# Kernel optimization log

Measured on AMD Instinct MI355X. Metric: run time of the kernel, lower is better.

The kernel has to match this reference:

```python
import jax, jax.numpy as jnp
import numpy as np

N, E, D_IN, D_HID, D_OUT = 50000, 800000, 64, 128, 64


def setup_inputs() -> dict:
    key = jax.random.key(0)
    ks = jax.random.split(key, 8)
    x = jax.random.normal(ks[0], (N, D_IN), dtype=jnp.float32)
    edge_index = jax.random.randint(ks[1], (2, E), 0, N, dtype=jnp.int64)
    # SAGEConv layer 1: lin_l (agg path, with bias), lin_r (root path, no bias)
    s1 = 1.0 / np.sqrt(D_IN)
    W_l1 = jax.random.uniform(ks[2], (D_HID, D_IN), jnp.float32, -s1, s1)
    b_l1 = jnp.zeros((D_HID,), jnp.float32)
    W_r1 = jax.random.uniform(ks[3], (D_HID, D_IN), jnp.float32, -s1, s1)
    s2 = 1.0 / np.sqrt(D_HID)
    W_l2 = jax.random.uniform(ks[4], (D_OUT, D_HID), jnp.float32, -s2, s2)
    b_l2 = jnp.zeros((D_OUT,), jnp.float32)
    W_r2 = jax.random.uniform(ks[5], (D_OUT, D_HID), jnp.float32, -s2, s2)
    return {"x": x, "edge_index": edge_index,
            "W_l1": W_l1, "b_l1": b_l1, "W_r1": W_r1,
            "W_l2": W_l2, "b_l2": b_l2, "W_r2": W_r2}


def _sage_layer(h, src, dst, W_l, b_l, W_r, n_nodes):
    # scatter-mean of source features onto targets
    msg = h[src]                                               # [E, d]
    summed = jax.ops.segment_sum(msg, dst, num_segments=n_nodes)
    deg = jax.ops.segment_sum(jnp.ones((src.shape[0], 1), h.dtype), dst,
                              num_segments=n_nodes)
    agg = summed / jnp.maximum(deg, 1.0)                       # [n, d]
    return agg @ W_l.T + b_l + h @ W_r.T


def reference(x, edge_index, W_l1, b_l1, W_r1, W_l2, b_l2, W_r2):
    src, dst = edge_index[0], edge_index[1]
    n = x.shape[0]
    h = _sage_layer(x, src, dst, W_l1, b_l1, W_r1, n)
    h = jnp.tanh(h)
    h = _sage_layer(h, src, dst, W_l2, b_l2, W_r2, n)
    return jax.nn.log_softmax(h, axis=1)
```

## Files before the change

### kernel.cpp

```cpp
#include <hip/hip_runtime.h>
#include <hip/hip_bf16.h>
#include <math.h>


typedef unsigned short u16;
typedef unsigned int   u32;
typedef __attribute__((ext_vector_type(8))) __bf16 bf16x8;
typedef __attribute__((ext_vector_type(4))) float  f32x4;

__device__ __forceinline__ u16 f2bf(float f) {
    u32 u = __float_as_uint(f);
    u32 r = (u + 0x7FFFu + ((u >> 16) & 1u)) >> 16;
    return (u16)r;
}
__device__ __forceinline__ float bfl(u32 u) { return __uint_as_float(u << 16); }
__device__ __forceinline__ float bfh(u32 u) { return __uint_as_float(u & 0xFFFF0000u); }
__device__ __forceinline__ u32 pack2(float a, float b) {
    return (u32)f2bf(a) | ((u32)f2bf(b) << 16);
}
__device__ __forceinline__ int pad16(int x) { return (x + 15) & ~15; }

__device__ __forceinline__ void fill_body(
    const int* __restrict__ src, const int* __restrict__ dst,
    int* __restrict__ cnt, u16* __restrict__ perm, int E, int N8,
    float invN8, int vb, int tid)
{
    int g = vb & 7;
    int e0 = (vb >> 3) * 2048 + tid * 8;
    int d[8];
    if (e0 + 8 <= E) {
        int4 d0 = *(const int4*)(dst + e0);
        int4 d1 = *(const int4*)(dst + e0 + 4);
        d[0] = d0.x; d[1] = d0.y; d[2] = d0.z; d[3] = d0.w;
        d[4] = d1.x; d[5] = d1.y; d[6] = d1.z; d[7] = d1.w;
    } else {
        for (int k = 0; k < 8; k++) d[k] = (e0 + k < E) ? dst[e0 + k] : -1;
    }
#pragma unroll
    for (int k = 0; k < 8; k++) {
        int dd = d[k];
        if (dd < 0) continue;
        int b = (int)((float)dd * invN8);
        if (dd >= (b + 1) * N8) b++;
        else if (dd < b * N8) b--;
        if (b != g) continue;
        int pos = atomicAdd(&cnt[dd], 1);
        if (pos < 64) perm[(size_t)dd * 64 + pos] = (u16)src[e0 + k];
    }
}

__global__ __launch_bounds__(256) void prep_kernel(
    const int* __restrict__ src, const int* __restrict__ dst,
    int* __restrict__ cnt, u16* __restrict__ perm, int E, int N8, float invN8,
    const float* __restrict__ x, uint4* __restrict__ xb4, int nCvt8,
    const float* __restrict__ Wl1, const float* __restrict__ Wr1,
    const float* __restrict__ Wl2, const float* __restrict__ Wr2,
    u16* __restrict__ W1c, u16* __restrict__ W2c,
    u16* __restrict__ xb, u16* __restrict__ m2b,
    int N, int FB, int VB)
{
    int blk = blockIdx.x, tid = threadIdx.x;
    if (blk < FB) {
        fill_body(src, dst, cnt, perm, E, N8, invN8, blk, tid);
    } else if (blk < FB + VB) {
        int i = (blk - FB) * 256 + tid;
        if (i < nCvt8) {
            float4 v0 = ((const float4*)x)[i * 2];
            float4 v1 = ((const float4*)x)[i * 2 + 1];
            uint4 p;
            p.x = pack2(v0.x, v0.y); p.y = pack2(v0.z, v0.w);
            p.z = pack2(v1.x, v1.y); p.w = pack2(v1.z, v1.w);
            xb4[i] = p;
        }
    } else if (blk < FB + VB + 64) {
        int i = (blk - FB - VB) * 256 + tid;
        if (i < 128 * 128) {
            int o = i >> 7, k = i & 127;
            float w1 = (k < 64) ? Wr1[o * 64 + k] : Wl1[o * 64 + (k - 64)];
            W1c[i] = f2bf(w1);
            float w2 = (o < 64) ? Wl2[o * 128 + k] : Wr2[(o - 64) * 128 + k];
            W2c[i] = f2bf(w2);
        }
    } else {
        if (tid < 32)      ((u32*)(xb  + (size_t)N * 64))[tid] = 0;
        else if (tid < 64) ((u32*)(m2b + (size_t)N * 64))[tid - 32] = 0;
    }
}

__device__ __forceinline__ void gather_wide(
    const u32* __restrict__ feat2, const u16* __restrict__ perm,
    int slot0, int degc, int pd, int rg, int c8, int lane, int N,
    float acc[8])
{
    float accB[8];
#pragma unroll
    for (int k = 0; k < 8; k++) { acc[k] = 0.f; accB[k] = 0.f; }
    int pidx = (int)perm[slot0 + lane];
    pidx = (lane < degc) ? pidx : N;
    for (int j = 0; j < pd; j += 16) {
        int rA = __shfl(pidx, j + rg,     64);
        int rB = __shfl(pidx, j + 8 + rg, 64);
        uint4 uA = *(const uint4*)(feat2 + (size_t)rA * 32 + c8 * 4);
        uint4 uB = *(const uint4*)(feat2 + (size_t)rB * 32 + c8 * 4);
        acc[0] += bfl(uA.x); acc[1] += bfh(uA.x);
        acc[2] += bfl(uA.y); acc[3] += bfh(uA.y);
        acc[4] += bfl(uA.z); acc[5] += bfh(uA.z);
        acc[6] += bfl(uA.w); acc[7] += bfh(uA.w);
        accB[0] += bfl(uB.x); accB[1] += bfh(uB.x);
        accB[2] += bfl(uB.y); accB[3] += bfh(uB.y);
        accB[4] += bfl(uB.z); accB[5] += bfh(uB.z);
        accB[6] += bfl(uB.w); accB[7] += bfh(uB.w);
    }
#pragma unroll
    for (int k = 0; k < 8; k++) acc[k] += accB[k];
#pragma unroll
    for (int k = 0; k < 8; k++) {
        acc[k] += __shfl_xor(acc[k], 8, 64);
        acc[k] += __shfl_xor(acc[k], 16, 64);
        acc[k] += __shfl_xor(acc[k], 32, 64);
    }
}

__global__ __launch_bounds__(512, 4) void gather_layer12_kernel(
    const u16* __restrict__ xb, const u16* __restrict__ perm,
    const int* __restrict__ cnt,
    const u16* __restrict__ W1, const float* __restrict__ b1,
    const u16* __restrict__ W2, const float* __restrict__ b2,
    u16* __restrict__ m2b, float* __restrict__ out, int N)
{
    __shared__ u16 agg_lds[64 * 64];
    __shared__ u16 tile4[4 * 2048];
    const int tid = threadIdx.x;
    const int wv = tid >> 6, lane = tid & 63;
    const int tb = blockIdx.x;

    {
        const int rg = lane >> 3, c8 = lane & 7;
#pragma unroll 2
        for (int i = 0; i < 8; i++) {
            int rr = wv * 8 + i;
            int nodec = min(tb * 64 + rr, N - 1);
            int deg = cnt[nodec];
            int degc = min(deg, 64);
            int pd = pad16(degc);
            float acc[8];
            gather_wide((const u32*)xb, perm, nodec * 64, degc, pd,
                        rg, c8, lane, N, acc);
            if (rg == 0) {
                float inv = 1.f / fmaxf((float)deg, 1.f);
                uint4 p;
                p.x = pack2(acc[0] * inv, acc[1] * inv);
                p.y = pack2(acc[2] * inv, acc[3] * inv);
                p.z = pack2(acc[4] * inv, acc[5] * inv);
                p.w = pack2(acc[6] * inv, acc[7] * inv);
                *(uint4*)&agg_lds[rr * 64 + ((c8 ^ (rr & 7)) << 3)] = p;
            }
        }
    }
    __syncthreads();

    const int quad = lane >> 4, l16 = lane & 15;
    u16* tile = tile4 + wv * 2048;
    bf16x8 a0, a1, a2, a3;
    if (wv < 4) {
        int node = tb * 64 + wv * 16 + l16;
        int nclamp = min(node, N - 1);
        const u16* xrow = xb + (size_t)nclamp * 64;
        a0 = *(const bf16x8*)(xrow + quad * 8);
        a1 = *(const bf16x8*)(xrow + 32 + quad * 8);
        int rr = wv * 16 + l16;
        a2 = *(const bf16x8*)&agg_lds[rr * 64 + ((quad       ^ (rr & 7)) << 3)];
        a3 = *(const bf16x8*)&agg_lds[rr * 64 + (((quad + 4) ^ (rr & 7)) << 3)];
#pragma unroll
        for (int nt = 0; nt < 8; nt++) {
            const u16* wrow = W1 + (size_t)(nt * 16 + l16) * 128 + quad * 8;
            f32x4 acc = {0.f, 0.f, 0.f, 0.f};
            acc = __builtin_amdgcn_mfma_f32_16x16x32_bf16(a0, *(const bf16x8*)(wrow),      acc, 0, 0, 0);
            acc = __builtin_amdgcn_mfma_f32_16x16x32_bf16(a1, *(const bf16x8*)(wrow + 32), acc, 0, 0, 0);
            acc = __builtin_amdgcn_mfma_f32_16x16x32_bf16(a2, *(const bf16x8*)(wrow + 64), acc, 0, 0, 0);
            acc = __builtin_amdgcn_mfma_f32_16x16x32_bf16(a3, *(const bf16x8*)(wrow + 96), acc, 0, 0, 0);
            int col = nt * 16 + l16;
            float bias = b1[col];
#pragma unroll
            for (int r = 0; r < 4; r++) {
                int row = quad * 4 + r;
                tile[row * 128 + (col ^ ((row & 7) << 3))] =
                    f2bf(tanhf(acc[r] + bias));
            }
        }
    }
    __syncthreads();

    if (wv < 4) {
        int swz = (l16 & 7) << 3;
        bf16x8 h0 = *(const bf16x8*)&tile[l16 * 128 + (( 0 + quad * 8) ^ swz)];
        bf16x8 h1 = *(const bf16x8*)&tile[l16 * 128 + ((32 + quad * 8) ^ swz)];
        bf16x8 h2 = *(const bf16x8*)&tile[l16 * 128 + ((64 + quad * 8) ^ swz)];
        bf16x8 h3 = *(const bf16x8*)&tile[l16 * 128 + ((96 + quad * 8) ^ swz)];
        int orow = tb * 64 + wv * 16 + quad * 4;
#pragma unroll
        for (int nt = 0; nt < 8; nt++) {
            const u16* wrow = W2 + (size_t)(nt * 16 + l16) * 128 + quad * 8;
            f32x4 acc = {0.f, 0.f, 0.f, 0.f};
            acc = __builtin_amdgcn_mfma_f32_16x16x32_bf16(h0, *(const bf16x8*)(wrow),      acc, 0, 0, 0);
            acc = __builtin_amdgcn_mfma_f32_16x16x32_bf16(h1, *(const bf16x8*)(wrow + 32), acc, 0, 0, 0);
            acc = __builtin_amdgcn_mfma_f32_16x16x32_bf16(h2, *(const bf16x8*)(wrow + 64), acc, 0, 0, 0);
            acc = __builtin_amdgcn_mfma_f32_16x16x32_bf16(h3, *(const bf16x8*)(wrow + 96), acc, 0, 0, 0);
            int oc = nt * 16 + l16;
#pragma unroll
            for (int r = 0; r < 4; r++) {
                int nn = orow + r;
                if (nn >= N) continue;
                if (oc < 64) m2b[(size_t)nn * 64 + oc] = f2bf(acc[r]);
                else         out[(size_t)nn * 64 + (oc - 64)] = acc[r] + b2[oc - 64];
            }
        }
    }
}

__global__ __launch_bounds__(256, 4) void gather2_final_kernel(
    const u32* __restrict__ m2b2, const u16* __restrict__ perm,
    const int* __restrict__ cnt, float* __restrict__ out, int N)
{
    int wid  = blockIdx.x * 4 + (threadIdx.x >> 6);
    int lane = threadIdx.x & 63;
    if (wid >= N) return;
    int deg = cnt[wid];
    int degc = min(deg, 64);
    int pd = pad16(degc);
    int rg = lane >> 3, c8 = lane & 7;
    float acc[8];
    gather_wide(m2b2, perm, wid * 64, degc, pd, rg, c8, lane, N, acc);
    float inv = 1.f / fmaxf((float)deg, 1.f);
    const float4* orow = (const float4*)(out + (size_t)wid * 64);
    float4 r20 = orow[c8 * 2];
    float4 r21 = orow[c8 * 2 + 1];
    float v[8];
    v[0] = acc[0] * inv + r20.x; v[1] = acc[1] * inv + r20.y;
    v[2] = acc[2] * inv + r20.z; v[3] = acc[3] * inv + r20.w;
    v[4] = acc[4] * inv + r21.x; v[5] = acc[5] * inv + r21.y;
    v[6] = acc[6] * inv + r21.z; v[7] = acc[7] * inv + r21.w;
    float m = v[0];
#pragma unroll
    for (int k = 1; k < 8; k++) m = fmaxf(m, v[k]);
#pragma unroll
    for (int o = 1; o < 8; o <<= 1) m = fmaxf(m, __shfl_xor(m, o, 64));
    float s = 0.f;
#pragma unroll
    for (int k = 0; k < 8; k++) s += expf(v[k] - m);
#pragma unroll
    for (int o = 1; o < 8; o <<= 1) s += __shfl_xor(s, o, 64);
    if (rg == 0) {
        float ls = m + logf(s);
        float4* ow = (float4*)(out + (size_t)wid * 64);
        ow[c8 * 2]     = make_float4(v[0] - ls, v[1] - ls, v[2] - ls, v[3] - ls);
        ow[c8 * 2 + 1] = make_float4(v[4] - ls, v[5] - ls, v[6] - ls, v[7] - ls);
    }
}

extern "C" void kernel_launch(void* const* d_in, const int* in_sizes, int n_in,
                              void* d_out, int out_size, void* d_ws, size_t ws_size,
                              hipStream_t stream)
{
    const float* x   = (const float*)d_in[0];
    const int*   ei  = (const int*)d_in[1];
    const float* Wl1 = (const float*)d_in[2];
    const float* bl1 = (const float*)d_in[3];
    const float* Wr1 = (const float*)d_in[4];
    const float* Wl2 = (const float*)d_in[5];
    const float* bl2 = (const float*)d_in[6];
    const float* Wr2 = (const float*)d_in[7];
    float* out = (float*)d_out;

    int N = in_sizes[0] / 64;
    int E = in_sizes[1] / 2;
    const int* src = ei;
    const int* dst = ei + E;
    int N8 = (N + 7) / 8;
    float invN8 = 1.0f / (float)N8;
    int chunks = (E + 2047) / 2048;
    int FB = chunks * 8;
    int nCvt8 = N * 64 / 8;
    int VB = (nCvt8 + 255) / 256;

    char* wsb = (char*)d_ws;
    size_t npad = ((size_t)N + 64) & ~(size_t)63;
    size_t permN = (size_t)N * 64;
    int* cnt  = (int*)wsb;
    u16* perm = (u16*)(cnt + npad);
    u16* xb   = perm + permN;
    u16* m2b  = xb + (size_t)(N + 1) * 64;
    u16* W1c  = m2b + (size_t)(N + 1) * 64;
    u16* W2c  = W1c + 128 * 128;

    hipMemsetAsync(cnt, 0, (size_t)N * sizeof(int), stream);

    prep_kernel<<<FB + VB + 64 + 1, 256, 0, stream>>>(
        src, dst, cnt, perm, E, N8, invN8,
        x, (uint4*)xb, nCvt8,
        Wl1, Wr1, Wl2, Wr2, W1c, W2c, xb, m2b, N, FB, VB);

    gather_layer12_kernel<<<(N + 63) / 64, 512, 0, stream>>>(
        xb, perm, cnt, W1c, bl1, W2c, bl2, m2b, out, N);

    gather2_final_kernel<<<(N + 3) / 4, 256, 0, stream>>>(
        (const u32*)m2b, perm, cnt, out, N);
}
```

Baseline: 200.4 us.

## Gather two nodes per wave and split MFMA tiles across all eight waves

The neighbour gather now handles two destination nodes per wave. Each lane reads its own perm index directly instead of using shuffles, and four feature-row loads are in flight per iteration, raising memory-level parallelism in both the layer-1 fused kernel and the final kernel. The dense MFMA phases of layer 1 and 2 are now split across all 8 waves, each taking half the output column tiles, instead of leaving 4 waves idle. The cost is more registers per lane and imbalanced loop trip counts when the two paired nodes have different degrees. Layer 1 now divides by the degree capped at 64 rather than the raw degree.

```diff
diff --git a/kernel.cpp b/kernel.cpp
--- a/kernel.cpp
+++ b/kernel.cpp
@@ -87,32 +87,47 @@
     }
 }
 
-__device__ __forceinline__ void gather_wide(
+__device__ __forceinline__ void gather_pair(
     const u32* __restrict__ feat2, const u16* __restrict__ perm,
-    int slot0, int degc, int pd, int rg, int c8, int lane, int N,
-    float acc[8])
-{
-    float accB[8];
-#pragma unroll
-    for (int k = 0; k < 8; k++) { acc[k] = 0.f; accB[k] = 0.f; }
-    int pidx = (int)perm[slot0 + lane];
-    pidx = (lane < degc) ? pidx : N;
-    for (int j = 0; j < pd; j += 16) {
-        int rA = __shfl(pidx, j + rg,     64);
-        int rB = __shfl(pidx, j + 8 + rg, 64);
-        uint4 uA = *(const uint4*)(feat2 + (size_t)rA * 32 + c8 * 4);
-        uint4 uB = *(const uint4*)(feat2 + (size_t)rB * 32 + c8 * 4);
-        acc[0] += bfl(uA.x); acc[1] += bfh(uA.x);
-        acc[2] += bfl(uA.y); acc[3] += bfh(uA.y);
-        acc[4] += bfl(uA.z); acc[5] += bfh(uA.z);
-        acc[6] += bfl(uA.w); acc[7] += bfh(uA.w);
-        accB[0] += bfl(uB.x); accB[1] += bfh(uB.x);
-        accB[2] += bfl(uB.y); accB[3] += bfh(uB.y);
-        accB[4] += bfl(uB.z); accB[5] += bfh(uB.z);
-        accB[6] += bfl(uB.w); accB[7] += bfh(uB.w);
-    }
-#pragma unroll
-    for (int k = 0; k < 8; k++) acc[k] += accB[k];
+    int nA, int nB, int degA, int degB, int rg, int c8, int N,
+    float accA[8], float accB[8])
+{
+#pragma unroll
+    for (int k = 0; k < 8; k++) { accA[k] = 0.f; accB[k] = 0.f; }
+    const u16* pA = perm + (size_t)nA * 64;
+    const u16* pB = perm + (size_t)nB * 64;
+    int pdmax = max(pad16(degA), pad16(degB));
+    for (int j = 0; j < pdmax; j += 16) {
+        int s0 = j + rg, s1 = j + 8 + rg;
+        int rA0 = (s0 < degA) ? (int)pA[s0] : N;
+        int rA1 = (s1 < degA) ? (int)pA[s1] : N;
+        int rB0 = (s0 < degB) ? (int)pB[s0] : N;
+        int rB1 = (s1 < degB) ? (int)pB[s1] : N;
+        uint4 uA0 = *(const uint4*)(feat2 + (size_t)rA0 * 32 + c8 * 4);
+        uint4 uA1 = *(const uint4*)(feat2 + (size_t)rA1 * 32 + c8 * 4);
+        uint4 uB0 = *(const uint4*)(feat2 + (size_t)rB0 * 32 + c8 * 4);
+        uint4 uB1 = *(const uint4*)(feat2 + (size_t)rB1 * 32 + c8 * 4);
+        accA[0] += bfl(uA0.x); accA[1] += bfh(uA0.x);
+        accA[2] += bfl(uA0.y); accA[3] += bfh(uA0.y);
+        accA[4] += bfl(uA0.z); accA[5] += bfh(uA0.z);
+        accA[6] += bfl(uA0.w); accA[7] += bfh(uA0.w);
+        accA[0] += bfl(uA1.x); accA[1] += bfh(uA1.x);
+        accA[2] += bfl(uA1.y); accA[3] += bfh(uA1.y);
+        accA[4] += bfl(uA1.z); accA[5] += bfh(uA1.z);
+        accA[6] += bfl(uA1.w); accA[7] += bfh(uA1.w);
+        accB[0] += bfl(uB0.x); accB[1] += bfh(uB0.x);
+        accB[2] += bfl(uB0.y); accB[3] += bfh(uB0.y);
+        accB[4] += bfl(uB0.z); accB[5] += bfh(uB0.z);
+        accB[6] += bfl(uB0.w); accB[7] += bfh(uB0.w);
+        accB[0] += bfl(uB1.x); accB[1] += bfh(uB1.x);
+        accB[2] += bfl(uB1.y); accB[3] += bfh(uB1.y);
+        accB[4] += bfl(uB1.z); accB[5] += bfh(uB1.z);
+        accB[6] += bfl(uB1.w); accB[7] += bfh(uB1.w);
+    }
+}
+
+__device__ __forceinline__ void reduce_rg(float acc[8])
+{
 #pragma unroll
     for (int k = 0; k < 8; k++) {
         acc[k] += __shfl_xor(acc[k], 8, 64);
@@ -136,43 +151,51 @@
 
     {
         const int rg = lane >> 3, c8 = lane & 7;
-#pragma unroll 2
-        for (int i = 0; i < 8; i++) {
-            int rr = wv * 8 + i;
-            int nodec = min(tb * 64 + rr, N - 1);
-            int deg = cnt[nodec];
-            int degc = min(deg, 64);
-            int pd = pad16(degc);
-            float acc[8];
-            gather_wide((const u32*)xb, perm, nodec * 64, degc, pd,
-                        rg, c8, lane, N, acc);
+        for (int i = 0; i < 8; i += 2) {
+            int rrA = wv * 8 + i, rrB = rrA + 1;
+            int nA = min(tb * 64 + rrA, N - 1);
+            int nB = min(tb * 64 + rrB, N - 1);
+            int degA = min(cnt[nA], 64), degB = min(cnt[nB], 64);
+            float accA[8], accB[8];
+            gather_pair((const u32*)xb, perm, nA, nB, degA, degB,
+                        rg, c8, N, accA, accB);
+            reduce_rg(accA);
+            reduce_rg(accB);
             if (rg == 0) {
-                float inv = 1.f / fmaxf((float)deg, 1.f);
-                uint4 p;
-                p.x = pack2(acc[0] * inv, acc[1] * inv);
-                p.y = pack2(acc[2] * inv, acc[3] * inv);
-                p.z = pack2(acc[4] * inv, acc[5] * inv);
-                p.w = pack2(acc[6] * inv, acc[7] * inv);
-                *(uint4*)&agg_lds[rr * 64 + ((c8 ^ (rr & 7)) << 3)] = p;
+                float invA = 1.f / fmaxf((float)degA, 1.f);
+                float invB = 1.f / fmaxf((float)degB, 1.f);
+                uint4 pa, pb;
+                pa.x = pack2(accA[0] * invA, accA[1] * invA);
+                pa.y = pack2(accA[2] * invA, accA[3] * invA);
+                pa.z = pack2(accA[4] * invA, accA[5] * invA);
+                pa.w = pack2(accA[6] * invA, accA[7] * invA);
+                pb.x = pack2(accB[0] * invB, accB[1] * invB);
+                pb.y = pack2(accB[2] * invB, accB[3] * invB);
+                pb.z = pack2(accB[4] * invB, accB[5] * invB);
+                pb.w = pack2(accB[6] * invB, accB[7] * invB);
+                *(uint4*)&agg_lds[rrA * 64 + ((c8 ^ (rrA & 7)) << 3)] = pa;
+                *(uint4*)&agg_lds[rrB * 64 + ((c8 ^ (rrB & 7)) << 3)] = pb;
             }
         }
     }
     __syncthreads();
 
     const int quad = lane >> 4, l16 = lane & 15;
-    u16* tile = tile4 + wv * 2048;
-    bf16x8 a0, a1, a2, a3;
-    if (wv < 4) {
-        int node = tb * 64 + wv * 16 + l16;
+    const int tIdx = wv & 3;
+    const int ntBase = (wv >> 2) * 4;
+    u16* tile = tile4 + tIdx * 2048;
+    {
+        int node = tb * 64 + tIdx * 16 + l16;
         int nclamp = min(node, N - 1);
         const u16* xrow = xb + (size_t)nclamp * 64;
-        a0 = *(const bf16x8*)(xrow + quad * 8);
-        a1 = *(const bf16x8*)(xrow + 32 + quad * 8);
-        int rr = wv * 16 + l16;
-        a2 = *(const bf16x8*)&agg_lds[rr * 64 + ((quad       ^ (rr & 7)) << 3)];
-        a3 = *(const bf16x8*)&agg_lds[rr * 64 + (((quad + 4) ^ (rr & 7)) << 3)];
-#pragma unroll
-        for (int nt = 0; nt < 8; nt++) {
+        bf16x8 a0 = *(const bf16x8*)(xrow + quad * 8);
+        bf16x8 a1 = *(const bf16x8*)(xrow + 32 + quad * 8);
+        int rr = tIdx * 16 + l16;
+        bf16x8 a2 = *(const bf16x8*)&agg_lds[rr * 64 + ((quad       ^ (rr & 7)) << 3)];
+        bf16x8 a3 = *(const bf16x8*)&agg_lds[rr * 64 + (((quad + 4) ^ (rr & 7)) << 3)];
+#pragma unroll
+        for (int t = 0; t < 4; t++) {
+            int nt = ntBase + t;
             const u16* wrow = W1 + (size_t)(nt * 16 + l16) * 128 + quad * 8;
             f32x4 acc = {0.f, 0.f, 0.f, 0.f};
             acc = __builtin_amdgcn_mfma_f32_16x16x32_bf16(a0, *(const bf16x8*)(wrow),      acc, 0, 0, 0);
@@ -191,15 +214,16 @@
     }
     __syncthreads();
 
-    if (wv < 4) {
+    {
         int swz = (l16 & 7) << 3;
         bf16x8 h0 = *(const bf16x8*)&tile[l16 * 128 + (( 0 + quad * 8) ^ swz)];
         bf16x8 h1 = *(const bf16x8*)&tile[l16 * 128 + ((32 + quad * 8) ^ swz)];
         bf16x8 h2 = *(const bf16x8*)&tile[l16 * 128 + ((64 + quad * 8) ^ swz)];
         bf16x8 h3 = *(const bf16x8*)&tile[l16 * 128 + ((96 + quad * 8) ^ swz)];
-        int orow = tb * 64 + wv * 16 + quad * 4;
-#pragma unroll
-        for (int nt = 0; nt < 8; nt++) {
+        int orow = tb * 64 + tIdx * 16 + quad * 4;
+#pragma unroll
+        for (int t = 0; t < 4; t++) {
+            int nt = ntBase + t;
             const u16* wrow = W2 + (size_t)(nt * 16 + l16) * 128 + quad * 8;
             f32x4 acc = {0.f, 0.f, 0.f, 0.f};
             acc = __builtin_amdgcn_mfma_f32_16x16x32_bf16(h0, *(const bf16x8*)(wrow),      acc, 0, 0, 0);
@@ -222,39 +246,61 @@
     const u32* __restrict__ m2b2, const u16* __restrict__ perm,
     const int* __restrict__ cnt, float* __restrict__ out, int N)
 {
-    int wid  = blockIdx.x * 4 + (threadIdx.x >> 6);
+    int widA = blockIdx.x * 8 + (threadIdx.x >> 6) * 2;
+    int widB = widA + 1;
     int lane = threadIdx.x & 63;
-    if (wid >= N) return;
-    int deg = cnt[wid];
-    int degc = min(deg, 64);
-    int pd = pad16(degc);
+    if (widA >= N) return;
+    int nA = widA, nB = min(widB, N - 1);
+    int degA = min(cnt[nA], 64), degB = min(cnt[nB], 64);
     int rg = lane >> 3, c8 = lane & 7;
-    float acc[8];
-    gather_wide(m2b2, perm, wid * 64, degc, pd, rg, c8, lane, N, acc);
-    float inv = 1.f / fmaxf((float)deg, 1.f);
-    const float4* orow = (const float4*)(out + (size_t)wid * 64);
-    float4 r20 = orow[c8 * 2];
-    float4 r21 = orow[c8 * 2 + 1];
-    float v[8];
-    v[0] = acc[0] * inv + r20.x; v[1] = acc[1] * inv + r20.y;
-    v[2] = acc[2] * inv + r20.z; v[3] = acc[3] * inv + r20.w;
-    v[4] = acc[4] * inv + r21.x; v[5] = acc[5] * inv + r21.y;
-    v[6] = acc[6] * inv + r21.z; v[7] = acc[7] * inv + r21.w;
-    float m = v[0];
-#pragma unroll
-    for (int k = 1; k < 8; k++) m = fmaxf(m, v[k]);
-#pragma unroll
-    for (int o = 1; o < 8; o <<= 1) m = fmaxf(m, __shfl_xor(m, o, 64));
-    float s = 0.f;
-#pragma unroll
-    for (int k = 0; k < 8; k++) s += expf(v[k] - m);
-#pragma unroll
-    for (int o = 1; o < 8; o <<= 1) s += __shfl_xor(s, o, 64);
+    const float4* orA = (const float4*)(out + (size_t)nA * 64);
+    const float4* orB = (const float4*)(out + (size_t)nB * 64);
+    float4 rA0 = orA[c8 * 2], rA1 = orA[c8 * 2 + 1];
+    float4 rB0 = orB[c8 * 2], rB1 = orB[c8 * 2 + 1];
+    float accA[8], accB[8];
+    gather_pair(m2b2, perm, nA, nB, degA, degB, rg, c8, N, accA, accB);
+    reduce_rg(accA);
+    reduce_rg(accB);
+
+    float invA = 1.f / fmaxf((float)cnt[nA], 1.f);
+    float invB = 1.f / fmaxf((float)cnt[nB], 1.f);
+    float vA[8], vB[8];
+    vA[0] = accA[0] * invA + rA0.x; vA[1] = accA[1] * invA + rA0.y;
+    vA[2] = accA[2] * invA + rA0.z; vA[3] = accA[3] * invA + rA0.w;
+    vA[4] = accA[4] * invA + rA1.x; vA[5] = accA[5] * invA + rA1.y;
+    vA[6] = accA[6] * invA + rA1.z; vA[7] = accA[7] * invA + rA1.w;
+    vB[0] = accB[0] * invB + rB0.x; vB[1] = accB[1] * invB + rB0.y;
+    vB[2] = accB[2] * invB + rB0.z; vB[3] = accB[3] * invB + rB0.w;
+    vB[4] = accB[4] * invB + rB1.x; vB[5] = accB[5] * invB + rB1.y;
+    vB[6] = accB[6] * invB + rB1.z; vB[7] = accB[7] * invB + rB1.w;
+
+    float mA = vA[0], mB = vB[0];
+#pragma unroll
+    for (int k = 1; k < 8; k++) { mA = fmaxf(mA, vA[k]); mB = fmaxf(mB, vB[k]); }
+#pragma unroll
+    for (int o = 1; o < 8; o <<= 1) {
+        mA = fmaxf(mA, __shfl_xor(mA, o, 64));
+        mB = fmaxf(mB, __shfl_xor(mB, o, 64));
+    }
+    float sA = 0.f, sB = 0.f;
+#pragma unroll
+    for (int k = 0; k < 8; k++) { sA += expf(vA[k] - mA); sB += expf(vB[k] - mB); }
+#pragma unroll
+    for (int o = 1; o < 8; o <<= 1) {
+        sA += __shfl_xor(sA, o, 64);
+        sB += __shfl_xor(sB, o, 64);
+    }
     if (rg == 0) {
-        float ls = m + logf(s);
-        float4* ow = (float4*)(out + (size_t)wid * 64);
-        ow[c8 * 2]     = make_float4(v[0] - ls, v[1] - ls, v[2] - ls, v[3] - ls);
-        ow[c8 * 2 + 1] = make_float4(v[4] - ls, v[5] - ls, v[6] - ls, v[7] - ls);
+        float lsA = mA + logf(sA);
+        float4* owA = (float4*)(out + (size_t)nA * 64);
+        owA[c8 * 2]     = make_float4(vA[0]-lsA, vA[1]-lsA, vA[2]-lsA, vA[3]-lsA);
+        owA[c8 * 2 + 1] = make_float4(vA[4]-lsA, vA[5]-lsA, vA[6]-lsA, vA[7]-lsA);
+        if (widB < N) {
+            float lsB = mB + logf(sB);
+            float4* owB = (float4*)(out + (size_t)nB * 64);
+            owB[c8 * 2]     = make_float4(vB[0]-lsB, vB[1]-lsB, vB[2]-lsB, vB[3]-lsB);
+            owB[c8 * 2 + 1] = make_float4(vB[4]-lsB, vB[5]-lsB, vB[6]-lsB, vB[7]-lsB);
+        }
     }
 }
 
@@ -303,6 +349,6 @@
     gather_layer12_kernel<<<(N + 63) / 64, 512, 0, stream>>>(
         xb, perm, cnt, W1c, bl1, W2c, bl2, m2b, out, N);
 
-    gather2_final_kernel<<<(N + 3) / 4, 256, 0, stream>>>(
+    gather2_final_kernel<<<(N + 7) / 8, 256, 0, stream>>>(
         (const u32*)m2b, perm, cnt, out, N);
 }
```

Measured after the change: 208.0 us. 3.8% more time.
